# Performance work log

Hardware: AMD Instinct MI355X
Metric: run time of the kernel (lower is better)

## Reference

```python
import jax, jax.numpy as jnp
import numpy as np

# --- module hyperparameters (init_kwargs) ---
IN_CH = 512
OUT_CH = 512
NUM_HEADS = 8
MODES = 64
LQ = 4096
LKV = 4096
E = IN_CH // NUM_HEADS      # per-head input dim = 64
EO = OUT_CH // NUM_HEADS    # per-head output dim = 64
B = 16

# mode_select_method='lowest' -> lowest-frequency modes, sorted (deterministic)
INDEX_Q = np.arange(min(MODES, LQ // 2))    # [Mq]
INDEX_KV = np.arange(min(MODES, LKV // 2))  # [Mkv]
SCALE = 1.0 / (IN_CH * OUT_CH)


def setup_inputs() -> dict:
    key = jax.random.key(0)
    kq, kk, kv, kw1, kw2 = jax.random.split(key, 5)
    return {
        "q": jax.random.normal(kq, (B, LQ, NUM_HEADS, E), jnp.float32),
        "k": jax.random.normal(kk, (B, LKV, NUM_HEADS, E), jnp.float32),
        "v": jax.random.normal(kv, (B, LKV, NUM_HEADS, E), jnp.float32),
        "weights1": SCALE * jax.random.normal(kw1, (NUM_HEADS, E, EO, len(INDEX_Q)), jnp.float32),
        "weights2": SCALE * jax.random.normal(kw2, (NUM_HEADS, E, EO, len(INDEX_Q)), jnp.float32),
    }


def reference(q, k, v, weights1, weights2):
    # q: [B, Lq, H, E]; k, v: [B, Lkv, H, E] (v is computed-but-unused in the
    # original forward; kept for signature fidelity).
    Bq, Lq, H, _ = q.shape
    xq = jnp.transpose(q, (0, 2, 3, 1))  # [B, H, E, Lq]
    xk = jnp.transpose(k, (0, 2, 3, 1))  # [B, H, E, Lkv]

    # rFFT along time, then gather the selected frequency modes
    xq_ft = jnp.fft.rfft(xq, axis=-1)[..., INDEX_Q]    # [B, H, E, Mq] complex
    xk_ft = jnp.fft.rfft(xk, axis=-1)[..., INDEX_KV]   # [B, H, E, Mkv] complex

    # complex cross-attention over modes (contract head-dim E)
    xqk = jnp.einsum('bhex,bhey->bhxy', xq_ft, xk_ft)  # [B, H, Mq, Mkv]
    # tanh applied independently to real/imag parts (as in compl activation)
    xqk = jax.lax.complex(jnp.tanh(xqk.real), jnp.tanh(xqk.imag))

    xqkv = jnp.einsum('bhxy,bhey->bhex', xqk, xk_ft)   # [B, H, E, Mq]

    w = jax.lax.complex(weights1, weights2)            # [H, E, EO, Mq]
    xqkvw = jnp.einsum('bhex,heox->bhox', xqkv, w)     # [B, H, EO, Mq]

    # scatter selected modes back into full half-spectrum, inverse FFT
    out_ft = jnp.zeros((Bq, H, EO, Lq // 2 + 1), jnp.complex64)
    out_ft = out_ft.at[..., INDEX_Q].set(xqkvw)
    out = jnp.fft.irfft(out_ft, n=Lq, axis=-1)         # [B, H, EO, Lq]

    out = jnp.transpose(out, (0, 3, 1, 2)) / (IN_CH * OUT_CH)  # [B, Lq, H, EO]
    return out
```

## Files before the change

### kernel.cpp

```cpp
#include <hip/hip_runtime.h>
#include <math.h>


constexpr float TWOPI_L = 1.5339807878856412e-3f;

typedef __attribute__((ext_vector_type(8))) short short8;
typedef __attribute__((ext_vector_type(4))) float f32x4;

__device__ __forceinline__ unsigned short f2bf(float f) {
    unsigned int u = __builtin_bit_cast(unsigned int, f);
    unsigned int r = (u + 0x7fffu + ((u >> 16) & 1u)) >> 16;
    return (unsigned short)r;
}
__device__ __forceinline__ float bf2f(unsigned short h) {
    unsigned int u = ((unsigned int)h) << 16;
    return __builtin_bit_cast(float, u);
}
__device__ __forceinline__ unsigned int cvtpk(float a, float b) {
    unsigned int r;
    asm("v_cvt_pk_bf16_f32 %0, %1, %2" : "=v"(r) : "v"(a), "v"(b));
    return r;
}
__device__ __forceinline__ void gld16(const float* g, void* l) {
    __builtin_amdgcn_global_load_lds(
        (const __attribute__((address_space(1))) void*)(g),
        (__attribute__((address_space(3))) void*)(l),
        16, 0, 0);
}
#define MSKR(r) (((((r) & 7)) << 1) | ((((r) >> 3)) & 1))

__global__ __launch_bounds__(256) void kprep(unsigned short* __restrict__ Whi,
                                             unsigned short* __restrict__ Wlo,
                                             const float* __restrict__ w1,
                                             const float* __restrict__ w2,
                                             float* __restrict__ wT)
{
    __shared__ float s1[64][65];
    __shared__ float s2[64][65];
    const int blk = blockIdx.x;
    const int tid = threadIdx.x;
    if (blk < 128) {
        const int idx = blk * 256 + tid;
        const int kt = idx >> 9;
        const int rb = (idx >> 6) & 7;
        const int l15 = (idx >> 2) & 15;
        const int lg = idx & 3;
        const int r_tab = rb * 16 + l15;
        int m, c;
        if (r_tab < 64) { m = (r_tab >> 1) * 2;              c = r_tab & 1; }
        else            { m = (((r_tab - 64) >> 1) * 2) + 1; c = r_tab & 1; }
        const int addr = (kt * 8 + rb) * 512 + l15 * 32 + lg * 8;
        unsigned short hbuf[8], lbuf[8];
#pragma unroll
        for (int j = 0; j < 8; ++j) {
            const int t = kt * 32 + lg * 8 + j;
            float sv, cv;
            sincosf((float)((m * t) & 4095) * TWOPI_L, &sv, &cv);
            const float v = c ? -sv : cv;
            const unsigned short hi = f2bf(v);
            hbuf[j] = hi;
            lbuf[j] = f2bf(v - bf2f(hi));
        }
        *(uint4*)(Whi + addr) = *(uint4*)hbuf;
        *(uint4*)(Wlo + addr) = *(uint4*)lbuf;
    } else {
        const int wblk = blk - 128;
        const int h = wblk >> 6, e = wblk & 63;
        const float* w1b = w1 + (size_t)(h * 64 + e) * 4096u;
        const float* w2b = w2 + (size_t)(h * 64 + e) * 4096u;
#pragma unroll
        for (int p = 0; p < 4; ++p) {
            const int f4 = tid + p * 256;
            const int o = f4 >> 4, m4 = (f4 & 15) * 4;
            *(float4*)&s1[o][m4] = *(const float4*)(w1b + f4 * 4);
            *(float4*)&s2[o][m4] = *(const float4*)(w2b + f4 * 4);
        }
        __syncthreads();
        float* dstb = wT + ((size_t)(h * 64) * 64u + (size_t)e) * 128u;
#pragma unroll
        for (int p = 0; p < 8; ++p) {
            const int f4 = tid + p * 256;
            const int m = f4 >> 5, c4 = f4 & 31;
            const int o = c4 * 2;
            const float4 v = make_float4(s1[o][m], s2[o][m], s1[o + 1][m], s2[o + 1][m]);
            *(float4*)(dstb + (size_t)m * 8192u + c4 * 4) = v;
        }
    }
}

__global__ __launch_bounds__(256, 2) void k1_mfma(const float* __restrict__ q,
                                                  const float* __restrict__ kin,
                                                  const unsigned short* __restrict__ Whi,
                                                  const unsigned short* __restrict__ Wlo,
                                                  float* __restrict__ Xq, float* __restrict__ Xk,
                                                  float* __restrict__ Pq, float* __restrict__ Pk)
{
    __shared__ float raw[3][64][64];
    __shared__ unsigned short xT[4][64][40];

    const int tid = threadIdx.x;
    const int bid = blockIdx.x;
    const int bh = bid >> 2, src = (bid >> 1) & 1, seg = bid & 1;
    const int b = bh >> 3, h = bh & 7;
    const float* __restrict__ x = src ? kin : q;
    const float* xb = x + (size_t)b * 2097152u + (size_t)h * 64u;

    const int wid = tid >> 6, lane = tid & 63;
    const int l15 = lane & 15, lg = lane >> 4;
    const int fp = (tid & 15) * 2;
    const int eqs = tid >> 4;
    const int sel = (wid >> 1) * 2;

    f32x4 acc[2][4];
#pragma unroll
    for (int mt = 0; mt < 2; ++mt)
#pragma unroll
        for (int nt = 0; nt < 4; ++nt)
            acc[mt][nt] = (f32x4){0.f, 0.f, 0.f, 0.f};

#define K1_STAGE(IT, BUF) do {                                                  \
    const int t0_ = (seg * 32 + ((IT) & 31)) * 32;                              \
    float* rbase_ = &raw[BUF][0][0];                                            \
    _Pragma("unroll")                                                           \
    for (int j = 0; j < 4; ++j) {                                               \
        const int c_ = wid * 4 + j;                                             \
        const int rl_ = 4 * c_ + (lane >> 4);                                   \
        const int t_ = t0_ + (rl_ & 31) + ((rl_ >> 5) << 11);                   \
        const int sq_ = (lane & 15) ^ MSKR(rl_);                                \
        gld16(xb + (size_t)t_ * 512u + (size_t)(sq_ * 4), rbase_ + c_ * 256);   \
    }                                                                           \
} while (0)

#define K1_ALOAD(IT, AH, AL) do {                                               \
    const int ksg_ = seg * 32 + ((IT) & 31);                                    \
    _Pragma("unroll")                                                           \
    for (int mt = 0; mt < 2; ++mt) {                                            \
        const size_t o_ = (size_t)((ksg_ * 8 + (wid * 2 + mt)) * 512 + l15 * 32 + lg * 8); \
        AH[mt] = *(const short8*)(Whi + o_);                                    \
        AL[mt] = *(const short8*)(Wlo + o_);                                    \
    }                                                                           \
} while (0)

#define K1_CONVERT(BUF) do {                                                    \
    const float* rb_ = &raw[BUF][0][0];                                         \
    float rs[16];                                                               \
    *(f32x4*)&rs[0]  = *(const f32x4*)(rb_ + (fp     ) * 64 + ((eqs ^ MSKR(fp))      * 4)); \
    *(f32x4*)&rs[4]  = *(const f32x4*)(rb_ + (fp + 1 ) * 64 + ((eqs ^ MSKR(fp + 1))  * 4)); \
    *(f32x4*)&rs[8]  = *(const f32x4*)(rb_ + (fp + 32) * 64 + ((eqs ^ MSKR(fp + 32)) * 4)); \
    *(f32x4*)&rs[12] = *(const f32x4*)(rb_ + (fp + 33) * 64 + ((eqs ^ MSKR(fp + 33)) * 4)); \
    _Pragma("unroll")                                                           \
    for (int ee = 0; ee < 4; ++ee) {                                            \
        const float a0 = rs[ee], a1 = rs[4 + ee];                               \
        const float c0 = rs[8 + ee], c1 = rs[12 + ee];                          \
        const float xp0 = a0 + c0, xp1 = a1 + c1;                               \
        const float xm0 = a0 - c0, xm1 = a1 - c1;                               \
        const int e_ = eqs * 4 + ee;                                            \
        const unsigned int php = cvtpk(xp0, xp1);                               \
        const float ph0 = __builtin_bit_cast(float, php << 16);                 \
        const float ph1 = __builtin_bit_cast(float, php & 0xffff0000u);         \
        const unsigned int plp = cvtpk(xp0 - ph0, xp1 - ph1);                   \
        const unsigned int mhp = cvtpk(xm0, xm1);                               \
        const float mh0 = __builtin_bit_cast(float, mhp << 16);                 \
        const float mh1 = __builtin_bit_cast(float, mhp & 0xffff0000u);         \
        const unsigned int mlp = cvtpk(xm0 - mh0, xm1 - mh1);                   \
        *(unsigned int*)&xT[0][e_][fp] = php;                                   \
        *(unsigned int*)&xT[1][e_][fp] = plp;                                   \
        *(unsigned int*)&xT[2][e_][fp] = mhp;                                   \
        *(unsigned int*)&xT[3][e_][fp] = mlp;                                   \
    }                                                                           \
} while (0)

#define K1_MFMA(AH, AL) do {                                                    \
    const unsigned short* sh = &xT[sel][0][0];                                  \
    const unsigned short* sl = &xT[sel + 1][0][0];                              \
    _Pragma("unroll")                                                           \
    for (int nt = 0; nt < 4; ++nt) {                                            \
        const int ri = (nt * 16 + l15) * 40 + 8 * lg;                           \
        const short8 Bh = *(const short8*)(sh + ri);                            \
        const short8 Bl = *(const short8*)(sl + ri);                            \
        _Pragma("unroll")                                                       \
        for (int mt = 0; mt < 2; ++mt)                                          \
            acc[mt][nt] = __builtin_amdgcn_mfma_f32_16x16x32_bf16(AH[mt], Bh, acc[mt][nt], 0, 0, 0); \
        _Pragma("unroll")                                                       \
        for (int mt = 0; mt < 2; ++mt)                                          \
            acc[mt][nt] = __builtin_amdgcn_mfma_f32_16x16x32_bf16(AH[mt], Bl, acc[mt][nt], 0, 0, 0); \
        _Pragma("unroll")                                                       \
        for (int mt = 0; mt < 2; ++mt)                                          \
            acc[mt][nt] = __builtin_amdgcn_mfma_f32_16x16x32_bf16(AL[mt], Bh, acc[mt][nt], 0, 0, 0); \
    }                                                                           \
} while (0)

    short8 AhA[2], AlA[2], AhB[2], AlB[2];
    K1_STAGE(0, 0);
    K1_ALOAD(0, AhA, AlA);
    K1_STAGE(1, 1);

    for (int itp = 0; itp < 16; ++itp) {
        const int it0 = 2 * itp;
        const int be = it0 % 3, bo = (it0 + 1) % 3;
        const int bs1 = (it0 + 2) % 3, bs2 = (it0 + 3) % 3;
        K1_ALOAD(it0 + 1, AhB, AlB);
        K1_STAGE(it0 + 2, bs1);
        __builtin_amdgcn_sched_barrier(0);
        asm volatile("s_waitcnt vmcnt(12)\n\ts_barrier" ::: "memory");
        K1_CONVERT(be);
        asm volatile("s_waitcnt lgkmcnt(0)\n\ts_barrier" ::: "memory");
        K1_MFMA(AhA, AlA);
        K1_ALOAD(it0 + 2, AhA, AlA);
        K1_STAGE(it0 + 3, bs2);
        __builtin_amdgcn_sched_barrier(0);
        asm volatile("s_waitcnt vmcnt(12)\n\ts_barrier" ::: "memory");
        K1_CONVERT(bo);
        asm volatile("s_waitcnt lgkmcnt(0)\n\ts_barrier" ::: "memory");
        K1_MFMA(AhB, AlB);
    }
    asm volatile("s_waitcnt vmcnt(0)" ::: "memory");

#undef K1_MFMA
#undef K1_CONVERT
#undef K1_ALOAD
#undef K1_STAGE

    float* Xd;
    if (seg == 0) Xd = src ? Xk : Xq;
    else          Xd = src ? Pk : Pq;
    Xd += (size_t)bh * 8192u;
    const int oddw = wid >> 1;
    const int wb = wid & 1;
#pragma unroll
    for (int mt = 0; mt < 2; ++mt) {
        const int r0 = (wb * 2 + mt) * 32 + 8 * lg + 2 * oddw;
#pragma unroll
        for (int nt = 0; nt < 4; ++nt) {
            const int e = nt * 16 + l15;
            *(float2*)(Xd + (size_t)e * 128u + r0) =
                make_float2(acc[mt][nt][0], acc[mt][nt][1]);
            *(float2*)(Xd + (size_t)e * 128u + r0 + 4) =
                make_float2(acc[mt][nt][2], acc[mt][nt][3]);
        }
    }
}

__global__ __launch_bounds__(256) void k2a_p1(const float* __restrict__ Xq,
                                              const float* __restrict__ Xk,
                                              const float* __restrict__ Pq,
                                              const float* __restrict__ Pk,
                                              float* __restrict__ P)
{
    const int blk = blockIdx.x;
    const int bh = blk >> 2, xt = blk & 3;
    __shared__ float sQ[64 * 32];
    __shared__ float sK[64 * 128];
    const int tid = threadIdx.x;
    const size_t boff = (size_t)bh * 8192u;

#pragma unroll
    for (int p = 0; p < 2; ++p) {
        const int f4 = tid + p * 256;
        const int row = f4 >> 3, c4 = f4 & 7;
        const size_t go = boff + (size_t)(row * 128 + xt * 32 + c4 * 4);
        const float4 a = *(const float4*)(Xq + go);
        const float4 b = *(const float4*)(Pq + go);
        *(float4*)&sQ[row * 32 + c4 * 4] =
            make_float4(a.x + b.x, a.y + b.y, a.z + b.z, a.w + b.w);
    }
#pragma unroll
    for (int p = 0; p < 8; ++p) {
        const int f4 = tid + p * 256;
        const float4 a = *(const float4*)(Xk + boff + (size_t)f4 * 4u);
        const float4 b = *(const float4*)(Pk + boff + (size_t)f4 * 4u);
        *(float4*)&sK[f4 * 4] =
            make_float4(a.x + b.x, a.y + b.y, a.z + b.z, a.w + b.w);
    }
    __syncthreads();

    const int xg = tid & 15, yg = tid >> 4;
    float aR[4] = {0.f, 0.f, 0.f, 0.f}, aI[4] = {0.f, 0.f, 0.f, 0.f};
#pragma unroll 8
    for (int e = 0; e < 64; ++e) {
        const float2 qv = *(const float2*)&sQ[e * 32 + 2 * xg];
        const float4 k0 = *(const float4*)&sK[e * 128 + 8 * yg];
        const float4 k1v = *(const float4*)&sK[e * 128 + 8 * yg + 4];
        aR[0] += qv.x * k0.x - qv.y * k0.y;   aI[0] += qv.x * k0.y + qv.y * k0.x;
        aR[1] += qv.x * k0.z - qv.y * k0.w;   aI[1] += qv.x * k0.w + qv.y * k0.z;
        aR[2] += qv.x * k1v.x - qv.y * k1v.y; aI[2] += qv.x * k1v.y + qv.y * k1v.x;
        aR[3] += qv.x * k1v.z - qv.y * k1v.w; aI[3] += qv.x * k1v.w + qv.y * k1v.z;
    }
    float* Pb = P + (size_t)bh * 8192u;
    const int x_abs = xt * 16 + xg;
#pragma unroll
    for (int j = 0; j < 4; ++j) {
        const int y = 4 * yg + j;
        *(float2*)(Pb + (size_t)y * 128u + 2 * x_abs) =
            make_float2(tanhf(aR[j]), tanhf(aI[j]));
    }
}

__global__ __launch_bounds__(256) void k2b_basis(const float* __restrict__ P,
                                                 const float* __restrict__ Xk,
                                                 const float* __restrict__ Pk,
                                                 float* __restrict__ PVG,
                                                 unsigned short* __restrict__ basis)
{
    __shared__ float sP[64 * 128];
    __shared__ float sKe[16 * 132];
    const int blk = blockIdx.x;
    const int tid = threadIdx.x;
    if (blk >= 512) {
        const int idx = (blk - 512) * 256 + tid;
        const int p0 = idx << 2;
        const int t = p0 >> 6;
        unsigned int pk[4];
#pragma unroll
        for (int j = 0; j < 4; ++j) {
            const int m = (p0 & 63) + j;
            float sv, cv;
            sincosf((float)((m * t) & 4095) * TWOPI_L, &sv, &cv);
            const float c = (m == 0) ? 1.0f : 2.0f * cv;
            const float s = (m == 0) ? 0.0f : -2.0f * sv;
            pk[j] = (unsigned int)f2bf(c) | ((unsigned int)f2bf(s) << 16);
        }
        *(uint4*)(basis + (size_t)t * 128u + ((p0 & 63) << 1)) =
            make_uint4(pk[0], pk[1], pk[2], pk[3]);
        return;
    }
    const int bh = blk >> 2, et = blk & 3;
    const int b = bh >> 3, h = bh & 7;
    const float* Pb = P + (size_t)bh * 8192u;
    const size_t koff = (size_t)bh * 8192u + (size_t)(et * 16) * 128u;

#pragma unroll
    for (int p = 0; p < 8; ++p) {
        const int f4 = tid + p * 256;
        *(float4*)&sP[f4 * 4] = *(const float4*)(Pb + f4 * 4);
    }
#pragma unroll
    for (int p = 0; p < 2; ++p) {
        const int f4 = tid + p * 256;
        const int row = f4 >> 5, c4 = f4 & 31;
        const size_t go = koff + (size_t)(row * 128 + c4 * 4);
        const float4 a = *(const float4*)(Xk + go);
        const float4 bb = *(const float4*)(Pk + go);
        *(float4*)&sKe[row * 132 + c4 * 4] =
            make_float4(a.x + bb.x, a.y + bb.y, a.z + bb.z, a.w + bb.w);
    }
    __syncthreads();

    const int xg = tid & 15, el = tid >> 4;
    float aR[4] = {0.f, 0.f, 0.f, 0.f}, aI[4] = {0.f, 0.f, 0.f, 0.f};
#pragma unroll 8
    for (int y = 0; y < 64; ++y) {
        const float2 kv = *(const float2*)&sKe[el * 132 + 2 * y];
        const float4 p0 = *(const float4*)&sP[y * 128 + 8 * xg];
        const float4 p1 = *(const float4*)&sP[y * 128 + 8 * xg + 4];
        aR[0] += p0.x * kv.x - p0.y * kv.y;   aI[0] += p0.x * kv.y + p0.y * kv.x;
        aR[1] += p0.z * kv.x - p0.w * kv.y;   aI[1] += p0.z * kv.y + p0.w * kv.x;
        aR[2] += p1.x * kv.x - p1.y * kv.y;   aI[2] += p1.x * kv.y + p1.y * kv.x;
        aR[3] += p1.z * kv.x - p1.w * kv.y;   aI[3] += p1.z * kv.y + p1.w * kv.x;
    }
    const int e_abs = et * 16 + el;
    float* base = PVG + (size_t)h * 131072u;
#pragma unroll
    for (int j = 0; j < 4; ++j) {
        const int m = 4 * xg + j;
        base[(size_t)m * 2048u + 0u    + (size_t)b * 64u + e_abs] = aR[j];
        base[(size_t)m * 2048u + 1024u + (size_t)b * 64u + e_abs] = aI[j];
    }
}

__global__ __launch_bounds__(256) void k2c_p4(const float* __restrict__ PVG,
                                              const float* __restrict__ wT,
                                              unsigned short* __restrict__ XWThi,
                                              unsigned short* __restrict__ XWTlo)
{
    const int blk = blockIdx.x;
    const int h = blk >> 6, m = blk & 63;
    __shared__ float sA[32 * 68];
    __shared__ float sW[64 * 128];
    const int tid = threadIdx.x;
    const float* Ab = PVG + (size_t)h * 131072u + (size_t)m * 2048u;
    const float* Wb = wT + ((size_t)h * 64u + m) * 8192u;

#pragma unroll
    for (int p = 0; p < 2; ++p) {
        const int f4 = tid + p * 256;
        const int row = f4 >> 4, e0 = (f4 & 15) * 4;
        *(float4*)&sA[row * 68 + e0] = *(const float4*)(Ab + row * 64 + e0);
    }
#pragma unroll
    for (int p = 0; p < 8; ++p) {
        const int f4 = tid + p * 256;
        *(float4*)&sW[f4 * 4] = *(const float4*)(Wb + f4 * 4);
    }
    __syncthreads();

    const int og = tid & 15, b = tid >> 4;
    float aR[4] = {0.f, 0.f, 0.f, 0.f}, aI[4] = {0.f, 0.f, 0.f, 0.f};
#pragma unroll 8
    for (int e = 0; e < 64; ++e) {
        const float pR = sA[b * 68 + e];
        const float pI = sA[(16 + b) * 68 + e];
        const float4 w0 = *(const float4*)&sW[e * 128 + 8 * og];
        const float4 w1v = *(const float4*)&sW[e * 128 + 8 * og + 4];
        aR[0] += pR * w0.x - pI * w0.y;   aI[0] += pR * w0.y + pI * w0.x;
        aR[1] += pR * w0.z - pI * w0.w;   aI[1] += pR * w0.w + pI * w0.z;
        aR[2] += pR * w1v.x - pI * w1v.y; aI[2] += pR * w1v.y + pI * w1v.x;
        aR[3] += pR * w1v.z - pI * w1v.w; aI[3] += pR * w1v.w + pI * w1v.z;
    }
    const int bh = b * 8 + h;
    unsigned short* Th = XWThi + (size_t)bh * 8192u;
    unsigned short* Tl = XWTlo + (size_t)bh * 8192u;
#pragma unroll
    for (int j = 0; j < 4; ++j) {
        const int o = 4 * og + j;
        const unsigned int hp = cvtpk(aR[j], aI[j]);
        const float hR = __builtin_bit_cast(float, hp << 16);
        const float hI = __builtin_bit_cast(float, hp & 0xffff0000u);
        const unsigned int lp = cvtpk(aR[j] - hR, aI[j] - hI);
        *(unsigned int*)(Th + (size_t)o * 128u + 2 * m) = hp;
        *(unsigned int*)(Tl + (size_t)o * 128u + 2 * m) = lp;
    }
}

__global__ __launch_bounds__(256, 3) void k3_mfma(const unsigned short* __restrict__ basis,
                                                  const unsigned short* __restrict__ XWThi,
                                                  const unsigned short* __restrict__ XWTlo,
                                                  float* __restrict__ out)
{
    const int bid = blockIdx.x;
    const int bh = bid >> 4, tc = bid & 15;
    const int b = bh >> 3, h = bh & 7;
    const int tid = threadIdx.x;
    const int wid = tid >> 6, lane = tid & 63;
    const int l15 = lane & 15, lg = lane >> 4;

    const int t0 = tc * 256 + wid * 64;
    const unsigned short* Th = XWThi + (size_t)bh * 8192u;
    const unsigned short* Tl = XWTlo + (size_t)bh * 8192u;

    f32x4 acc[4][4];
#pragma unroll
    for (int mt = 0; mt < 4; ++mt)
#pragma unroll
        for (int nt = 0; nt < 4; ++nt)
            acc[mt][nt] = (f32x4){0.f, 0.f, 0.f, 0.f};

#pragma unroll
    for (int ks = 0; ks < 4; ++ks) {
        const int ko = ks * 32 + 8 * lg;
        short8 A[4], Bh[4], Bl[4];
#pragma unroll
        for (int mt = 0; mt < 4; ++mt)
            A[mt] = *(const short8*)(basis + (size_t)(t0 + mt * 16 + l15) * 128u + ko);
#pragma unroll
        for (int nt = 0; nt < 4; ++nt) {
            Bh[nt] = *(const short8*)(Th + (size_t)(nt * 16 + l15) * 128u + ko);
            Bl[nt] = *(const short8*)(Tl + (size_t)(nt * 16 + l15) * 128u + ko);
        }
#pragma unroll
        for (int mt = 0; mt < 4; ++mt)
#pragma unroll
            for (int nt = 0; nt < 4; ++nt)
                acc[mt][nt] = __builtin_amdgcn_mfma_f32_16x16x32_bf16(A[mt], Bh[nt], acc[mt][nt], 0, 0, 0);
#pragma unroll
        for (int mt = 0; mt < 4; ++mt)
#pragma unroll
            for (int nt = 0; nt < 4; ++nt)
                acc[mt][nt] = __builtin_amdgcn_mfma_f32_16x16x32_bf16(A[mt], Bl[nt], acc[mt][nt], 0, 0, 0);
    }

    const float scale = 9.313225746154785e-10f;
#pragma unroll
    for (int mt = 0; mt < 4; ++mt)
#pragma unroll
        for (int nt = 0; nt < 4; ++nt) {
            const int o = nt * 16 + l15;
#pragma unroll
            for (int j = 0; j < 4; ++j) {
                const int t = t0 + mt * 16 + 4 * lg + j;
                out[((size_t)(b * 4096 + t) * 8u + (size_t)h) * 64u + o] = acc[mt][nt][j] * scale;
            }
        }
}

extern "C" void kernel_launch(void* const* d_in, const int* in_sizes, int n_in,
                              void* d_out, int out_size, void* d_ws, size_t ws_size,
                              hipStream_t stream) {
    (void)in_sizes; (void)n_in; (void)out_size; (void)ws_size;
    const float* q  = (const float*)d_in[0];
    const float* k  = (const float*)d_in[1];
    const float* w1 = (const float*)d_in[3];
    const float* w2 = (const float*)d_in[4];
    float* out = (float*)d_out;

    float* ws = (float*)d_ws;
    float* Xq = ws;
    float* Xk = ws + 1048576;
    unsigned short* XWThi = (unsigned short*)(ws + 2097152);
    unsigned short* XWTlo = XWThi + 1048576;
    unsigned short* basis = (unsigned short*)ws;

    unsigned short* Whi = (unsigned short*)out;
    unsigned short* Wlo = Whi + 262144;
    float* Pq  = out + 524288;
    float* Pk  = out + 1572864;
    float* P   = out + 16777216;
    float* wT  = out + 17825792;
    float* PVG = out + 22020096;

    hipLaunchKernelGGL(kprep,     dim3(640),  dim3(256), 0, stream, Whi, Wlo, w1, w2, wT);
    hipLaunchKernelGGL(k1_mfma,   dim3(512),  dim3(256), 0, stream, q, k, Whi, Wlo, Xq, Xk, Pq, Pk);
    hipLaunchKernelGGL(k2a_p1,    dim3(512),  dim3(256), 0, stream, Xq, Xk, Pq, Pk, P);
    hipLaunchKernelGGL(k2b_basis, dim3(768),  dim3(256), 0, stream, P, Xk, Pk, PVG, basis);
    hipLaunchKernelGGL(k2c_p4,    dim3(512),  dim3(256), 0, stream, PVG, wT, XWThi, XWTlo);
    hipLaunchKernelGGL(k3_mfma,   dim3(2048), dim3(256), 0, stream, basis, XWThi, XWTlo, out);
}
```

Before: 188.9 us.

## Process q and k in the same k1 block and split time into four segments

```diff
diff --git a/kernel.cpp b/kernel.cpp
--- a/kernel.cpp
+++ b/kernel.cpp
@@ -100,10 +100,10 @@
 
     const int tid = threadIdx.x;
     const int bid = blockIdx.x;
-    const int bh = bid >> 2, src = (bid >> 1) & 1, seg = bid & 1;
+    const int bh = bid >> 2, seg = bid & 3;
     const int b = bh >> 3, h = bh & 7;
-    const float* __restrict__ x = src ? kin : q;
-    const float* xb = x + (size_t)b * 2097152u + (size_t)h * 64u;
+    const float* xqb = q   + (size_t)b * 2097152u + (size_t)h * 64u;
+    const float* xkb = kin + (size_t)b * 2097152u + (size_t)h * 64u;
 
     const int wid = tid >> 6, lane = tid & 63;
     const int l15 = lane & 15, lg = lane >> 4;
@@ -111,15 +111,19 @@
     const int eqs = tid >> 4;
     const int sel = (wid >> 1) * 2;
 
-    f32x4 acc[2][4];
+    f32x4 accQ[2][4], accK[2][4];
 #pragma unroll
     for (int mt = 0; mt < 2; ++mt)
 #pragma unroll
-        for (int nt = 0; nt < 4; ++nt)
-            acc[mt][nt] = (f32x4){0.f, 0.f, 0.f, 0.f};
-
-#define K1_STAGE(IT, BUF) do {                                                  \
-    const int t0_ = (seg * 32 + ((IT) & 31)) * 32;                              \
+        for (int nt = 0; nt < 4; ++nt) {
+            accQ[mt][nt] = (f32x4){0.f, 0.f, 0.f, 0.f};
+            accK[mt][nt] = (f32x4){0.f, 0.f, 0.f, 0.f};
+        }
+
+#define K1_STAGE(SLOT, BUF) do {                                                \
+    const int sl_ = (SLOT) & 31;                                                \
+    const float* xb_ = (sl_ & 1) ? xkb : xqb;                                   \
+    const int t0_ = (seg * 16 + (sl_ >> 1)) * 32;                               \
     float* rbase_ = &raw[BUF][0][0];                                            \
     _Pragma("unroll")                                                           \
     for (int j = 0; j < 4; ++j) {                                               \
@@ -127,12 +131,12 @@
         const int rl_ = 4 * c_ + (lane >> 4);                                   \
         const int t_ = t0_ + (rl_ & 31) + ((rl_ >> 5) << 11);                   \
         const int sq_ = (lane & 15) ^ MSKR(rl_);                                \
-        gld16(xb + (size_t)t_ * 512u + (size_t)(sq_ * 4), rbase_ + c_ * 256);   \
+        gld16(xb_ + (size_t)t_ * 512u + (size_t)(sq_ * 4), rbase_ + c_ * 256);  \
     }                                                                           \
 } while (0)
 
-#define K1_ALOAD(IT, AH, AL) do {                                               \
-    const int ksg_ = seg * 32 + ((IT) & 31);                                    \
+#define K1_ALOAD(I, AH, AL) do {                                                \
+    const int ksg_ = seg * 16 + ((I) & 15);                                     \
     _Pragma("unroll")                                                           \
     for (int mt = 0; mt < 2; ++mt) {                                            \
         const size_t o_ = (size_t)((ksg_ * 8 + (wid * 2 + mt)) * 512 + l15 * 32 + lg * 8); \
@@ -170,7 +174,7 @@
     }                                                                           \
 } while (0)
 
-#define K1_MFMA(AH, AL) do {                                                    \
+#define K1_MFMA(ACC, AH, AL) do {                                               \
     const unsigned short* sh = &xT[sel][0][0];                                  \
     const unsigned short* sl = &xT[sel + 1][0][0];                              \
     _Pragma("unroll")                                                           \
@@ -180,14 +184,33 @@
         const short8 Bl = *(const short8*)(sl + ri);                            \
         _Pragma("unroll")                                                       \
         for (int mt = 0; mt < 2; ++mt)                                          \
-            acc[mt][nt] = __builtin_amdgcn_mfma_f32_16x16x32_bf16(AH[mt], Bh, acc[mt][nt], 0, 0, 0); \
+            ACC[mt][nt] = __builtin_amdgcn_mfma_f32_16x16x32_bf16(AH[mt], Bh, ACC[mt][nt], 0, 0, 0); \
         _Pragma("unroll")                                                       \
         for (int mt = 0; mt < 2; ++mt)                                          \
-            acc[mt][nt] = __builtin_amdgcn_mfma_f32_16x16x32_bf16(AH[mt], Bl, acc[mt][nt], 0, 0, 0); \
+            ACC[mt][nt] = __builtin_amdgcn_mfma_f32_16x16x32_bf16(AH[mt], Bl, ACC[mt][nt], 0, 0, 0); \
         _Pragma("unroll")                                                       \
         for (int mt = 0; mt < 2; ++mt)                                          \
-            acc[mt][nt] = __builtin_amdgcn_mfma_f32_16x16x32_bf16(AL[mt], Bh, acc[mt][nt], 0, 0, 0); \
+            ACC[mt][nt] = __builtin_amdgcn_mfma_f32_16x16x32_bf16(AL[mt], Bh, ACC[mt][nt], 0, 0, 0); \
     }                                                                           \
+} while (0)
+
+#define K1_PAIR(PAIRI, AH, AL, NAH, NAL) do {                                   \
+    const int s0_ = 2 * (PAIRI);                                                \
+                                                                    \
+    K1_ALOAD((PAIRI) + 1, NAH, NAL);                                            \
+    K1_STAGE(s0_ + 2, (s0_ + 2) % 3);                                           \
+    __builtin_amdgcn_sched_barrier(0);                                          \
+    asm volatile("s_waitcnt vmcnt(12)\n\ts_barrier" ::: "memory");              \
+    K1_CONVERT(s0_ % 3);                                                        \
+    asm volatile("s_waitcnt lgkmcnt(0)\n\ts_barrier" ::: "memory");             \
+    K1_MFMA(accQ, AH, AL);                                                      \
+                                                                    \
+    K1_STAGE(s0_ + 3, (s0_ + 3) % 3);                                           \
+    __builtin_amdgcn_sched_barrier(0);                                          \
+    asm volatile("s_waitcnt vmcnt(12)\n\ts_barrier" ::: "memory");              \
+    K1_CONVERT((s0_ + 1) % 3);                                                  \
+    asm volatile("s_waitcnt lgkmcnt(0)\n\ts_barrier" ::: "memory");             \
+    K1_MFMA(accK, AH, AL);                                                      \
 } while (0)
 
     short8 AhA[2], AlA[2], AhB[2], AlB[2];
@@ -195,36 +218,22 @@
     K1_ALOAD(0, AhA, AlA);
     K1_STAGE(1, 1);
 
-    for (int itp = 0; itp < 16; ++itp) {
-        const int it0 = 2 * itp;
-        const int be = it0 % 3, bo = (it0 + 1) % 3;
-        const int bs1 = (it0 + 2) % 3, bs2 = (it0 + 3) % 3;
-        K1_ALOAD(it0 + 1, AhB, AlB);
-        K1_STAGE(it0 + 2, bs1);
-        __builtin_amdgcn_sched_barrier(0);
-        asm volatile("s_waitcnt vmcnt(12)\n\ts_barrier" ::: "memory");
-        K1_CONVERT(be);
-        asm volatile("s_waitcnt lgkmcnt(0)\n\ts_barrier" ::: "memory");
-        K1_MFMA(AhA, AlA);
-        K1_ALOAD(it0 + 2, AhA, AlA);
-        K1_STAGE(it0 + 3, bs2);
-        __builtin_amdgcn_sched_barrier(0);
-        asm volatile("s_waitcnt vmcnt(12)\n\ts_barrier" ::: "memory");
-        K1_CONVERT(bo);
-        asm volatile("s_waitcnt lgkmcnt(0)\n\ts_barrier" ::: "memory");
-        K1_MFMA(AhB, AlB);
+    for (int pp = 0; pp < 8; ++pp) {
+        K1_PAIR(2 * pp,     AhA, AlA, AhB, AlB);
+        K1_PAIR(2 * pp + 1, AhB, AlB, AhA, AlA);
     }
     asm volatile("s_waitcnt vmcnt(0)" ::: "memory");
 
+#undef K1_PAIR
 #undef K1_MFMA
 #undef K1_CONVERT
 #undef K1_ALOAD
 #undef K1_STAGE
 
-    float* Xd;
-    if (seg == 0) Xd = src ? Xk : Xq;
-    else          Xd = src ? Pk : Pq;
-    Xd += (size_t)bh * 8192u;
+    float* Xdq = (seg == 0) ? Xq : (Pq + (size_t)(seg - 1) * 1048576u);
+    float* Xdk = (seg == 0) ? Xk : (Pk + (size_t)(seg - 1) * 1048576u);
+    Xdq += (size_t)bh * 8192u;
+    Xdk += (size_t)bh * 8192u;
     const int oddw = wid >> 1;
     const int wb = wid & 1;
 #pragma unroll
@@ -233,10 +242,14 @@
 #pragma unroll
         for (int nt = 0; nt < 4; ++nt) {
             const int e = nt * 16 + l15;
-            *(float2*)(Xd + (size_t)e * 128u + r0) =
-                make_float2(acc[mt][nt][0], acc[mt][nt][1]);
-            *(float2*)(Xd + (size_t)e * 128u + r0 + 4) =
-                make_float2(acc[mt][nt][2], acc[mt][nt][3]);
+            *(float2*)(Xdq + (size_t)e * 128u + r0) =
+                make_float2(accQ[mt][nt][0], accQ[mt][nt][1]);
+            *(float2*)(Xdq + (size_t)e * 128u + r0 + 4) =
+                make_float2(accQ[mt][nt][2], accQ[mt][nt][3]);
+            *(float2*)(Xdk + (size_t)e * 128u + r0) =
+                make_float2(accK[mt][nt][0], accK[mt][nt][1]);
+            *(float2*)(Xdk + (size_t)e * 128u + r0 + 4) =
+                make_float2(accK[mt][nt][2], accK[mt][nt][3]);
         }
     }
 }
@@ -259,18 +272,25 @@
         const int f4 = tid + p * 256;
         const int row = f4 >> 3, c4 = f4 & 7;
         const size_t go = boff + (size_t)(row * 128 + xt * 32 + c4 * 4);
-        const float4 a = *(const float4*)(Xq + go);
-        const float4 b = *(const float4*)(Pq + go);
-        *(float4*)&sQ[row * 32 + c4 * 4] =
-            make_float4(a.x + b.x, a.y + b.y, a.z + b.z, a.w + b.w);
+        float4 a = *(const float4*)(Xq + go);
+#pragma unroll
+        for (int s = 0; s < 3; ++s) {
+            const float4 bb = *(const float4*)(Pq + (size_t)s * 1048576u + go);
+            a.x += bb.x; a.y += bb.y; a.z += bb.z; a.w += bb.w;
+        }
+        *(float4*)&sQ[row * 32 + c4 * 4] = a;
     }
 #pragma unroll
     for (int p = 0; p < 8; ++p) {
         const int f4 = tid + p * 256;
-        const float4 a = *(const float4*)(Xk + boff + (size_t)f4 * 4u);
-        const float4 b = *(const float4*)(Pk + boff + (size_t)f4 * 4u);
-        *(float4*)&sK[f4 * 4] =
-            make_float4(a.x + b.x, a.y + b.y, a.z + b.z, a.w + b.w);
+        const size_t go = boff + (size_t)f4 * 4u;
+        float4 a = *(const float4*)(Xk + go);
+#pragma unroll
+        for (int s = 0; s < 3; ++s) {
+            const float4 bb = *(const float4*)(Pk + (size_t)s * 1048576u + go);
+            a.x += bb.x; a.y += bb.y; a.z += bb.z; a.w += bb.w;
+        }
+        *(float4*)&sK[f4 * 4] = a;
     }
     __syncthreads();
 
@@ -339,10 +359,13 @@
         const int f4 = tid + p * 256;
         const int row = f4 >> 5, c4 = f4 & 31;
         const size_t go = koff + (size_t)(row * 128 + c4 * 4);
-        const float4 a = *(const float4*)(Xk + go);
-        const float4 bb = *(const float4*)(Pk + go);
-        *(float4*)&sKe[row * 132 + c4 * 4] =
-            make_float4(a.x + bb.x, a.y + bb.y, a.z + bb.z, a.w + bb.w);
+        float4 a = *(const float4*)(Xk + go);
+#pragma unroll
+        for (int s = 0; s < 3; ++s) {
+            const float4 bb = *(const float4*)(Pk + (size_t)s * 1048576u + go);
+            a.x += bb.x; a.y += bb.y; a.z += bb.z; a.w += bb.w;
+        }
+        *(float4*)&sKe[row * 132 + c4 * 4] = a;
     }
     __syncthreads();
 
@@ -503,7 +526,7 @@
     unsigned short* Whi = (unsigned short*)out;
     unsigned short* Wlo = Whi + 262144;
     float* Pq  = out + 524288;
-    float* Pk  = out + 1572864;
+    float* Pk  = out + 3670016;
     float* P   = out + 16777216;
     float* wT  = out + 17825792;
     float* PVG = out + 22020096;
```

Measured after the change: 200.9 us. 6.3% more time.
